# Kernel optimization log

Measured on AMD Instinct MI355X. Metric: run time of the kernel, lower is better.

The kernel has to match this reference:

```python
import jax, jax.numpy as jnp
import numpy as np

B, LTMS, TTS, C_IN, F, H = 64, 16, 256, 128, 256, 256


def setup_inputs() -> dict:
    key = jax.random.key(0)
    ks = jax.random.split(key, 6)
    s = 0.05  # small init keeps relu-GRU numerically tame
    return {
        "x": jax.random.normal(ks[0], (B, LTMS * TTS, C_IN), dtype=jnp.float32),
        "conv_w": jax.random.normal(ks[1], (1, C_IN, F), dtype=jnp.float32) * s,
        "conv_b": jnp.zeros((F,), dtype=jnp.float32),
        "attn_w": jax.random.normal(ks[2], (TTS, TTS), dtype=jnp.float32) * s,
        "attn_b": jnp.zeros((TTS,), dtype=jnp.float32),
        "gru_w": jax.random.normal(ks[3], (F, 3 * H), dtype=jnp.float32) * s,
        "gru_u": jax.random.normal(ks[4], (H, 3 * H), dtype=jnp.float32) * s,
        "gru_b": jnp.zeros((2, 3 * H), dtype=jnp.float32),
    }


def _forward(x, conv_w, conv_b, attn_w, attn_b, gru_w, gru_u, gru_b):
    b = x.shape[0]
    # [B, LTMS*TTS, C] -> [B*LTMS, TTS, C]; segments are independent, so the
    # original per-segment Python loop vectorizes into the leading batch dim.
    xs = x.reshape(b * LTMS, TTS, C_IN)
    # Conv1D kernel_size=1 == pointwise GEMM, then ReLU (dropout=0 at inference)
    conv = jax.nn.relu(jnp.einsum('ntc,cf->ntf', xs, conv_w[0]) + conv_b)  # [N,T,F]
    # Attention: softmax(Dense) over time axis per filter, multiply back
    xt = conv.transpose(0, 2, 1)                                  # [N,F,T]
    probs = jax.nn.softmax(xt @ attn_w + attn_b, axis=-1)         # [N,F,T]
    x_att = conv * probs.transpose(0, 2, 1)                       # [N,T,F]
    # GRU (keras v2, reset_after=True), activation=relu, gate order z,r,h
    bi, br = gru_b[0], gru_b[1]
    gates_x = x_att @ gru_w + bi                                  # [N,T,3H]
    def step(h, gx):
        rec = h @ gru_u + br
        xz, xr, xh = jnp.split(gx, 3, axis=-1)
        rz, rr, rh = jnp.split(rec, 3, axis=-1)
        z = jax.nn.sigmoid(xz + rz)
        r = jax.nn.sigmoid(xr + rr)
        hh = jax.nn.relu(xh + r * rh)
        h_new = z * h + (1.0 - z) * hh
        return h_new, None
    h0 = jnp.zeros((b * LTMS, H), dtype=x.dtype)
    h_final, _ = jax.lax.scan(step, h0, gates_x.transpose(1, 0, 2))
    return h_final.reshape(b, LTMS, H)


def reference(x, conv_w, conv_b, attn_w, attn_b, gru_w, gru_u, gru_b):
    return _forward(x, conv_w, conv_b, attn_w, attn_b, gru_w, gru_u, gru_b)
```

## Files before the change

kernel.cpp:

```cpp
#include <hip/hip_runtime.h>
#include <stdint.h>

typedef unsigned short u16;
typedef __attribute__((ext_vector_type(8))) __bf16 bf16x8;
typedef __attribute__((ext_vector_type(8))) u16 u16x8;
typedef __attribute__((ext_vector_type(4))) float f32x4;

#define TTS 256
#define NSEG 1024
#define TC 32

__device__ __forceinline__ u16 f2bf(float f) {
  union { float f; uint32_t u; } v; v.f = f;
  uint32_t r = v.u + 0x7fffu + ((v.u >> 16) & 1u);
  return (u16)(r >> 16);
}
__device__ __forceinline__ float bf2f(u16 h) {
  union { uint32_t u; float f; } v; v.u = ((uint32_t)h) << 16;
  return v.f;
}
__device__ __forceinline__ float sigm(float x) {
  return __builtin_amdgcn_rcpf(1.0f + __expf(-x));
}
__device__ __forceinline__ void gl16(const void* g, void* l) {
  __builtin_amdgcn_global_load_lds(
      (const __attribute__((address_space(1))) unsigned int*)g,
      (__attribute__((address_space(3))) unsigned int*)l, 16, 0, 0);
}

__global__ void k_transp4(const float* __restrict__ cw, const float* __restrict__ aw,
                          const float* __restrict__ gw, const float* __restrict__ gu,
                          u16* __restrict__ cwT, u16* __restrict__ awT,
                          u16* __restrict__ gwT, u16* __restrict__ guT) {
  int b = blockIdx.x;
  const float* in; u16* out; int R, C, base;
  if (b < 128)       { in = cw; out = cwT; R = 128; C = 256; base = 0; }
  else if (b < 384)  { in = aw; out = awT; R = 256; C = 256; base = 128; }
  else if (b < 1152) { in = gw; out = gwT; R = 256; C = 768; base = 384; }
  else               { in = gu; out = guT; R = 256; C = 768; base = 1152; }
  int i = (b - base) * 256 + threadIdx.x;
  if (i < R * C) {
    int r = i / C, c = i % C;
    out[(size_t)c * R + r] = f2bf(in[i]);
  }
}

template <bool RELU, bool STORE_T, int AMODE>
__global__ __launch_bounds__(512, 2) void k_gemm(
    const void* __restrict__ Av, const u16* __restrict__ Bt,
    const float* __restrict__ bias, u16* __restrict__ out, int K, int Nld, int t0) {
  __shared__ __attribute__((aligned(16))) u16 ldsA[2][4096];
  __shared__ __attribute__((aligned(16))) u16 ldsB[2][8192];
  __shared__ __attribute__((aligned(16))) u16 xw[STORE_T ? 8 * 16 * 70 : 16];
  const int tid  = threadIdx.x;
  const int w    = tid >> 6;
  const int lane = tid & 63;
  const int quad = lane >> 4;
  const int l16  = lane & 15;
  const int m0 = blockIdx.x * 128;
  const int n0 = blockIdx.y * 256;
  const int wm = w >> 2, wn = w & 3;
  const int srow = tid >> 2;
  const int scs  = (tid & 3) ^ (srow & 3);
  const int aslot = (srow * 4 + scs) * 8;
  const int xsw  = (quad ^ (l16 & 3)) * 8;
  const float* Af = (const float*)Av;
  const u16*   Ax = (const u16*)Av;

  f32x4 acc[4][4];
#pragma unroll
  for (int i = 0; i < 4; i++)
#pragma unroll
    for (int j = 0; j < 4; j++) acc[i][j] = f32x4{0.f, 0.f, 0.f, 0.f};

  float4 p0, p1;
  if (AMODE == 0) {
    const float* p = Af + (size_t)(m0 + srow) * K + (tid & 3) * 8;
    p0 = *(const float4*)p;
    p1 = *(const float4*)(p + 4);
  } else {
    int r = m0 + srow, kk = scs * 8;
    gl16(Ax + (size_t)(r >> 5) * 65536 + (size_t)(kk >> 6) * 16384 +
             (t0 + (r & 31)) * 64 + (kk & 63),
         &ldsA[0][tid * 8]);
  }
#pragma unroll
  for (int i = 0; i < 2; i++) {
    int idx = i * 512 + tid, brow = idx >> 2;
    int bcs = (idx & 3) ^ (brow & 3);
    gl16(Bt + (size_t)(n0 + brow) * K + bcs * 8, &ldsB[0][idx * 8]);
  }
  if (AMODE == 0) {
    *(ushort4*)&ldsA[0][aslot]     = ushort4{f2bf(p0.x), f2bf(p0.y), f2bf(p0.z), f2bf(p0.w)};
    *(ushort4*)&ldsA[0][aslot + 4] = ushort4{f2bf(p1.x), f2bf(p1.y), f2bf(p1.z), f2bf(p1.w)};
  }
  __syncthreads();

  int cur = 0;
  for (int k0 = 0; k0 < K; k0 += 32) {
    const int kn = k0 + 32;
    const bool more = kn < K;
    float4 q0, q1;
    if (more) {
      if (AMODE == 0) {
        const float* p = Af + (size_t)(m0 + srow) * K + kn + (tid & 3) * 8;
        q0 = *(const float4*)p;
        q1 = *(const float4*)(p + 4);
      } else {
        int r = m0 + srow, kk = kn + scs * 8;
        gl16(Ax + (size_t)(r >> 5) * 65536 + (size_t)(kk >> 6) * 16384 +
                 (t0 + (r & 31)) * 64 + (kk & 63),
             &ldsA[cur ^ 1][tid * 8]);
      }
#pragma unroll
      for (int i = 0; i < 2; i++) {
        int idx = i * 512 + tid, brow = idx >> 2;
        int bcs = (idx & 3) ^ (brow & 3);
        gl16(Bt + (size_t)(n0 + brow) * K + kn + bcs * 8, &ldsB[cur ^ 1][idx * 8]);
      }
    }
    bf16x8 a[4], b[4];
#pragma unroll
    for (int i = 0; i < 4; i++)
      a[i] = *(const bf16x8*)&ldsA[cur][(wm * 64 + i * 16 + l16) * 32 + xsw];
#pragma unroll
    for (int j = 0; j < 4; j++)
      b[j] = *(const bf16x8*)&ldsB[cur][(wn * 64 + j * 16 + l16) * 32 + xsw];
#pragma unroll
    for (int i = 0; i < 4; i++)
#pragma unroll
      for (int j = 0; j < 4; j++)
        acc[i][j] = __builtin_amdgcn_mfma_f32_16x16x32_bf16(a[i], b[j], acc[i][j], 0, 0, 0);
    if (AMODE == 0 && more) {
      *(ushort4*)&ldsA[cur ^ 1][aslot]     = ushort4{f2bf(q0.x), f2bf(q0.y), f2bf(q0.z), f2bf(q0.w)};
      *(ushort4*)&ldsA[cur ^ 1][aslot + 4] = ushort4{f2bf(q1.x), f2bf(q1.y), f2bf(q1.z), f2bf(q1.w)};
    }
    __syncthreads();
    cur ^= 1;
  }

  if (STORE_T) {
    const int nseg = m0 >> 8;
    const int ttw  = (m0 & 255) + wm * 64;
    const int col16 = lane >> 2, part = lane & 3;
    u16* xwp = &xw[w * 16 * 70];
#pragma unroll
    for (int j = 0; j < 4; j++) {
      int col = n0 + wn * 64 + j * 16 + l16;
      float bv = bias[col];
#pragma unroll
      for (int i = 0; i < 4; i++)
#pragma unroll
        for (int r = 0; r < 4; r++) {
          float v = acc[i][j][r] + bv;
          if (RELU) v = fmaxf(v, 0.f);
          xwp[l16 * 70 + i * 16 + quad * 4 + r] = f2bf(v);
        }
      u16x8 v0 = *(const u16x8*)&xwp[col16 * 70 + part * 16];
      u16x8 v1 = *(const u16x8*)&xwp[col16 * 70 + part * 16 + 8];
      int colS = n0 + wn * 64 + j * 16 + col16;
      size_t ob = (size_t)nseg * 65536 + (size_t)(colS >> 6) * 16384 +
                  (size_t)(colS & 63) * 256 + ttw + part * 16;
      *(u16x8*)&out[ob]     = v0;
      *(u16x8*)&out[ob + 8] = v1;
    }
  } else {
#pragma unroll
    for (int j = 0; j < 4; j++) {
      int col = n0 + wn * 64 + j * 16 + l16;
      float bv = bias[col];
#pragma unroll
      for (int i = 0; i < 4; i++) {
        int row0 = m0 + wm * 64 + i * 16 + quad * 4;
#pragma unroll
        for (int r = 0; r < 4; r++) {
          float v = acc[i][j][r] + bv;
          if (RELU) v = fmaxf(v, 0.f);
          out[(size_t)(row0 + r) * Nld + col] = f2bf(v);
        }
      }
    }
  }
}

__global__ __launch_bounds__(256, 3) void k_attn(
    u16* xac,
    const u16* __restrict__ Wt,
    const float* __restrict__ attn_b) {
  __shared__ __attribute__((aligned(16))) u16 ldsC[16384];
  __shared__ float redmax[4][64];
  __shared__ float redsum[4][64];
  __shared__ __attribute__((aligned(16))) u16 xbuf[4][16][76];
  const int tid  = threadIdx.x;
  const int w    = tid >> 6;
  const int lane = tid & 63;
  const int quad = lane >> 4;
  const int l16  = lane & 15;
  const int seg = blockIdx.x;
  const int c4  = blockIdx.y;
  u16* reg = xac + (size_t)seg * 65536 + (size_t)c4 * 16384;

#pragma unroll
  for (int u = 0; u < 8; u++) {
    int id = u * 256 + tid;
    int f = id >> 5;
    gl16(reg + ((id * 8) ^ ((f & 7) << 3)), &ldsC[id * 8]);
  }
  __syncthreads();

  f32x4 acc[4][4];
#pragma unroll
  for (int i = 0; i < 4; i++)
#pragma unroll
    for (int j = 0; j < 4; j++) acc[i][j] = f32x4{0.f, 0.f, 0.f, 0.f};

#pragma unroll
  for (int s = 0; s < 8; s++) {
    int k0 = s * 32;
    bf16x8 a[4], b[4];
#pragma unroll
    for (int i = 0; i < 4; i++)
      a[i] = *(const bf16x8*)(Wt + (size_t)(w * 64 + i * 16 + l16) * 256 + k0 + quad * 8);
#pragma unroll
    for (int j = 0; j < 4; j++) {
      int fl = j * 16 + l16;
      b[j] = *(const bf16x8*)&ldsC[(fl * 256 + s * 32 + quad * 8) ^ ((fl & 7) << 3)];
    }
#pragma unroll
    for (int i = 0; i < 4; i++)
#pragma unroll
      for (int j = 0; j < 4; j++)
        acc[i][j] = __builtin_amdgcn_mfma_f32_16x16x32_bf16(a[i], b[j], acc[i][j], 0, 0, 0);
  }

#pragma unroll
  for (int i = 0; i < 4; i++)
#pragma unroll
    for (int r = 0; r < 4; r++) {
      float ab = attn_b[w * 64 + i * 16 + quad * 4 + r];
#pragma unroll
      for (int j = 0; j < 4; j++) acc[i][j][r] += ab;
    }

  float lmax[4];
#pragma unroll
  for (int j = 0; j < 4; j++) {
    float m = -1e30f;
#pragma unroll
    for (int i = 0; i < 4; i++)
#pragma unroll
      for (int r = 0; r < 4; r++) m = fmaxf(m, acc[i][j][r]);
    m = fmaxf(m, __shfl_xor(m, 16));
    m = fmaxf(m, __shfl_xor(m, 32));
    lmax[j] = m;
  }
  if (quad == 0) {
#pragma unroll
    for (int j = 0; j < 4; j++) redmax[w][j * 16 + l16] = lmax[j];
  }
  __syncthreads();
  float gmax[4];
#pragma unroll
  for (int j = 0; j < 4; j++) {
    int c = j * 16 + l16;
    gmax[j] = fmaxf(fmaxf(redmax[0][c], redmax[1][c]), fmaxf(redmax[2][c], redmax[3][c]));
  }
  float lsum[4];
#pragma unroll
  for (int j = 0; j < 4; j++) {
    float sacc = 0.f;
#pragma unroll
    for (int i = 0; i < 4; i++)
#pragma unroll
      for (int r = 0; r < 4; r++) {
        float e = __expf(acc[i][j][r] - gmax[j]);
        acc[i][j][r] = e;
        sacc += e;
      }
    sacc += __shfl_xor(sacc, 16);
    sacc += __shfl_xor(sacc, 32);
    lsum[j] = sacc;
  }
  if (quad == 0) {
#pragma unroll
    for (int j = 0; j < 4; j++) redsum[w][j * 16 + l16] = lsum[j];
  }
  __syncthreads();
  float rinv[4];
#pragma unroll
  for (int j = 0; j < 4; j++) {
    int c = j * 16 + l16;
    rinv[j] = 1.0f / (redsum[0][c] + redsum[1][c] + redsum[2][c] + redsum[3][c]);
  }

#pragma unroll
  for (int i = 0; i < 4; i++) {
#pragma unroll
    for (int r = 0; r < 4; r++) {
      int tp = w * 64 + i * 16 + quad * 4 + r;
#pragma unroll
      for (int j = 0; j < 4; j++) {
        int fl = j * 16 + l16;
        float cv = bf2f(ldsC[(fl * 256 + tp) ^ ((fl & 7) << 3)]);
        float xa = acc[i][j][r] * rinv[j] * cv;
        xbuf[w][quad * 4 + r][fl] = f2bf(xa);
      }
    }
    int rr = lane >> 2, oc = lane & 3;
    u16x8 v0 = *(const u16x8*)&xbuf[w][rr][oc * 16];
    u16x8 v1 = *(const u16x8*)&xbuf[w][rr][oc * 16 + 8];
    int tpb = w * 64 + i * 16 + rr;
    *(u16x8*)&reg[(size_t)tpb * 64 + oc * 16]     = v0;
    *(u16x8*)&reg[(size_t)tpb * 64 + oc * 16 + 8] = v1;
  }
}

__global__ __launch_bounds__(512) __attribute__((amdgpu_waves_per_eu(2, 2)))
void k_scan(
    const u16* __restrict__ gc,
    const u16* __restrict__ Ut,
    const float* __restrict__ br,
    float* __restrict__ hio,
    int init) {
  __shared__ __attribute__((aligned(16))) u16 hbT[2][4096];
  __shared__ __attribute__((aligned(16))) u16 ldsG[2][12288];
  const int tid  = threadIdx.x;
  const int w    = tid >> 6;
  const int lane = tid & 63;
  const int quad = lane >> 4;
  const int l16  = lane & 15;
  const int n0 = blockIdx.x * 16;
  const int cg[2] = {w, 8 + w};

  bf16x8 U[2][3][8];
#pragma unroll
  for (int grp = 0; grp < 2; grp++)
#pragma unroll
    for (int g = 0; g < 3; g++)
#pragma unroll
      for (int s = 0; s < 8; s++) {
        U[grp][g][s] = *(const bf16x8*)(Ut + (size_t)(g * 256 + cg[grp] * 16 + l16) * 256 + s * 32 + quad * 8);
        asm volatile("" : "+v"(U[grp][g][s]));
      }

  float brZ[2], brR[2], brH[2];
#pragma unroll
  for (int grp = 0; grp < 2; grp++) {
    int c = cg[grp] * 16 + l16;
    brZ[grp] = br[c]; brR[grp] = br[256 + c]; brH[grp] = br[512 + c];
  }

  int gbase[2], hwb[2];
#pragma unroll
  for (int grp = 0; grp < 2; grp++) {
    gbase[grp] = cg[grp] * 256 + quad * 16 + l16;
    int c = cg[grp] * 16 + l16;
    hwb[grp] = (c >> 5) * 512 + ((c >> 3) & 3) * 128 + (c & 7) + quad * 32;
  }
  const int ahb = quad * 128 + l16 * 8;

  float hreg[2][4];
#pragma unroll
  for (int grp = 0; grp < 2; grp++)
#pragma unroll
    for (int r = 0; r < 4; r++) {
      hreg[grp][r] = init ? 0.f
                          : hio[(size_t)(n0 + quad * 4 + r) * 256 + cg[grp] * 16 + l16];
      hbT[0][hwb[grp] + r * 8] = f2bf(hreg[grp][r]);
    }

  const u16* sp[3];
#pragma unroll
  for (int k = 0; k < 3; k++) {
    int id = tid + k * 512;
    int a = id & 1, q = (id >> 1) & 3, r = (id >> 3) & 3;
    int cgv = (id >> 5) & 15, g = id >> 9;
    sp[k] = gc + ((size_t)(n0 + q * 4 + r) * 32 + 0) * 768 + g * 256 + cgv * 16 + a * 8;
  }
#pragma unroll
  for (int k = 0; k < 3; k++) {
    gl16(sp[k], &ldsG[0][(tid + k * 512) * 8]);
    sp[k] += 768;
  }
  __syncthreads();

  for (int tt = 0; tt < TC; tt++) {
    if (tt + 1 < TC) {
#pragma unroll
      for (int k = 0; k < 3; k++) {
        gl16(sp[k], &ldsG[(tt + 1) & 1][(tid + k * 512) * 8]);
        sp[k] += 768;
      }
    }

    f32x4 acc[2][3];
#pragma unroll
    for (int grp = 0; grp < 2; grp++)
#pragma unroll
      for (int g = 0; g < 3; g++) acc[grp][g] = f32x4{0.f, 0.f, 0.f, 0.f};

    const u16* hR = hbT[tt & 1];
#pragma unroll
    for (int s = 0; s < 8; s++) {
      bf16x8 ah = *(const bf16x8*)&hR[ahb + s * 512];
#pragma unroll
      for (int grp = 0; grp < 2; grp++)
#pragma unroll
        for (int g = 0; g < 3; g++)
          acc[grp][g] = __builtin_amdgcn_mfma_f32_16x16x32_bf16(ah, U[grp][g][s], acc[grp][g], 0, 0, 0);
    }

    const u16* G = ldsG[tt & 1];
    u16* hW = hbT[(tt + 1) & 1];
#pragma unroll
    for (int grp = 0; grp < 2; grp++)
#pragma unroll
      for (int r = 0; r < 4; r++) {
        float gz = bf2f(G[gbase[grp] + 0 * 4096 + r * 64]);
        float gr = bf2f(G[gbase[grp] + 1 * 4096 + r * 64]);
        float gh = bf2f(G[gbase[grp] + 2 * 4096 + r * 64]);
        float z  = sigm(acc[grp][0][r] + gz + brZ[grp]);
        float rg = sigm(acc[grp][1][r] + gr + brR[grp]);
        float hh = fmaxf(gh + rg * (acc[grp][2][r] + brH[grp]), 0.f);
        float hn = z * hreg[grp][r] + (1.0f - z) * hh;
        hreg[grp][r] = hn;
        hW[hwb[grp] + r * 8] = f2bf(hn);
      }
    __syncthreads();
  }

#pragma unroll
  for (int grp = 0; grp < 2; grp++)
#pragma unroll
    for (int r = 0; r < 4; r++)
      hio[(size_t)(n0 + quad * 4 + r) * 256 + cg[grp] * 16 + l16] = hreg[grp][r];
}

extern "C" void kernel_launch(void* const* d_in, const int* in_sizes, int n_in,
                              void* d_out, int out_size, void* d_ws, size_t ws_size,
                              hipStream_t stream) {
  (void)in_sizes; (void)n_in; (void)out_size;
  const float* x      = (const float*)d_in[0];
  const float* conv_w = (const float*)d_in[1];
  const float* conv_b = (const float*)d_in[2];
  const float* attn_w = (const float*)d_in[3];
  const float* attn_b = (const float*)d_in[4];
  const float* gru_w  = (const float*)d_in[5];
  const float* gru_u  = (const float*)d_in[6];
  const float* gru_b  = (const float*)d_in[7];

  const size_t NEEDED = 185532416;
  if (ws_size < NEEDED) return;
  char* ws = (char*)d_ws;
  u16* xac     = (u16*)(ws);
  u16* gatesC  = (u16*)(ws + 134217728);
  u16* conv_wT = (u16*)(ws + 184549376);
  u16* attn_wT = (u16*)(ws + 184614912);
  u16* gru_wT  = (u16*)(ws + 184745984);
  u16* gru_uT  = (u16*)(ws + 185139200);

  hipLaunchKernelGGL(k_transp4, dim3(1920), dim3(256), 0, stream,
                     conv_w, attn_w, gru_w, gru_u, conv_wT, attn_wT, gru_wT, gru_uT);

  hipLaunchKernelGGL((k_gemm<true, true, 0>), dim3(2048, 1), dim3(512), 0, stream,
                     (const void*)x, conv_wT, conv_b, xac, 128, 0, 0);
  hipLaunchKernelGGL(k_attn, dim3(1024, 4), dim3(256), 0, stream,
                     xac, attn_wT, attn_b);
  for (int c = 0; c < 8; c++) {
    hipLaunchKernelGGL((k_gemm<false, false, 1>), dim3(256, 3), dim3(512), 0, stream,
                       (const void*)xac, gru_wT, gru_b, gatesC, 256, 768, c * TC);
    hipLaunchKernelGGL(k_scan, dim3(64), dim3(512), 0, stream,
                       gatesC, gru_uT, gru_b + 768, (float*)d_out, c == 0 ? 1 : 0);
  }
}
```

Baseline: 1.122 ms.

## Deepen scan gate prefetch to 3 stages with explicit vmcnt waits and swizzled layout

The GRU scan kernel's gate prefetch ring grows from double to quadruple buffering, running three timesteps ahead. The plain __syncthreads is replaced by explicit vmcnt/lgkmcnt waits plus s_barrier, so loads still in flight need not drain every step. The gate tile is now copied row-contiguously with an XOR swizzle to cut LDS bank conflicts on reads. The attention launch is also split into two half-grid launches, which adds launch overhead without an obvious benefit.

```diff
diff --git a/kernel.cpp b/kernel.cpp
--- a/kernel.cpp
+++ b/kernel.cpp
@@ -9,6 +9,10 @@
 #define TTS 256
 #define NSEG 1024
 #define TC 32
+
+#define WAITV(N) asm volatile("s_waitcnt vmcnt(" #N ")" ::: "memory")
+#define LGKM0    asm volatile("s_waitcnt lgkmcnt(0)" ::: "memory")
+#define SBAR     do { __builtin_amdgcn_s_barrier(); __builtin_amdgcn_sched_barrier(0); } while (0)
 
 __device__ __forceinline__ u16 f2bf(float f) {
   union { float f; uint32_t u; } v; v.f = f;
@@ -186,7 +190,7 @@
 __global__ __launch_bounds__(256, 3) void k_attn(
     u16* xac,
     const u16* __restrict__ Wt,
-    const float* __restrict__ attn_b) {
+    const float* __restrict__ attn_b, int seg0) {
   __shared__ __attribute__((aligned(16))) u16 ldsC[16384];
   __shared__ float redmax[4][64];
   __shared__ float redsum[4][64];
@@ -196,7 +200,7 @@
   const int lane = tid & 63;
   const int quad = lane >> 4;
   const int l16  = lane & 15;
-  const int seg = blockIdx.x;
+  const int seg = blockIdx.x + seg0;
   const int c4  = blockIdx.y;
   u16* reg = xac + (size_t)seg * 65536 + (size_t)c4 * 16384;
 
@@ -323,7 +327,7 @@
     float* __restrict__ hio,
     int init) {
   __shared__ __attribute__((aligned(16))) u16 hbT[2][4096];
-  __shared__ __attribute__((aligned(16))) u16 ldsG[2][12288];
+  __shared__ __attribute__((aligned(16))) u16 ldsG[4][12288];
   const int tid  = threadIdx.x;
   const int w    = tid >> 6;
   const int lane = tid & 63;
@@ -350,10 +354,10 @@
     brZ[grp] = br[c]; brR[grp] = br[256 + c]; brH[grp] = br[512 + c];
   }
 
-  int gbase[2], hwb[2];
+  int csw[2], hwb[2];
 #pragma unroll
   for (int grp = 0; grp < 2; grp++) {
-    gbase[grp] = cg[grp] * 256 + quad * 16 + l16;
+    csw[grp] = (cg[grp] * 16 + l16) ^ (quad << 4);
     int c = cg[grp] * 16 + l16;
     hwb[grp] = (c >> 5) * 512 + ((c >> 3) & 3) * 128 + (c & 7) + quad * 32;
   }
@@ -373,22 +377,27 @@
 #pragma unroll
   for (int k = 0; k < 3; k++) {
     int id = tid + k * 512;
-    int a = id & 1, q = (id >> 1) & 3, r = (id >> 3) & 3;
-    int cgv = (id >> 5) & 15, g = id >> 9;
-    sp[k] = gc + ((size_t)(n0 + q * 4 + r) * 32 + 0) * 768 + g * 256 + cgv * 16 + a * 8;
-  }
-#pragma unroll
-  for (int k = 0; k < 3; k++) {
-    gl16(sp[k], &ldsG[0][(tid + k * 512) * 8]);
-    sp[k] += 768;
-  }
-  __syncthreads();
+    int row = id / 96, col16 = id - row * 96;
+    int sw = ((row >> 2) & 3) << 4;
+    sp[k] = gc + (size_t)(n0 + row) * TC * 768 + ((col16 * 8) ^ sw);
+  }
+#pragma unroll
+  for (int p = 0; p < 3; p++) {
+#pragma unroll
+    for (int k = 0; k < 3; k++) {
+      gl16(sp[k], &ldsG[p][(tid + k * 512) * 8]);
+      sp[k] += 768;
+    }
+  }
+  WAITV(6);
+  LGKM0;
+  SBAR;
 
   for (int tt = 0; tt < TC; tt++) {
-    if (tt + 1 < TC) {
+    if (tt < TC - 3) {
 #pragma unroll
       for (int k = 0; k < 3; k++) {
-        gl16(sp[k], &ldsG[(tt + 1) & 1][(tid + k * 512) * 8]);
+        gl16(sp[k], &ldsG[(tt + 3) & 3][(tid + k * 512) * 8]);
         sp[k] += 768;
       }
     }
@@ -410,15 +419,16 @@
           acc[grp][g] = __builtin_amdgcn_mfma_f32_16x16x32_bf16(ah, U[grp][g][s], acc[grp][g], 0, 0, 0);
     }
 
-    const u16* G = ldsG[tt & 1];
+    const u16* G = ldsG[tt & 3];
     u16* hW = hbT[(tt + 1) & 1];
 #pragma unroll
     for (int grp = 0; grp < 2; grp++)
 #pragma unroll
       for (int r = 0; r < 4; r++) {
-        float gz = bf2f(G[gbase[grp] + 0 * 4096 + r * 64]);
-        float gr = bf2f(G[gbase[grp] + 1 * 4096 + r * 64]);
-        float gh = bf2f(G[gbase[grp] + 2 * 4096 + r * 64]);
+        int rb = (quad * 4 + r) * 768 + csw[grp];
+        float gz = bf2f(G[rb]);
+        float gr = bf2f(G[rb + 256]);
+        float gh = bf2f(G[rb + 512]);
         float z  = sigm(acc[grp][0][r] + gz + brZ[grp]);
         float rg = sigm(acc[grp][1][r] + gr + brR[grp]);
         float hh = fmaxf(gh + rg * (acc[grp][2][r] + brH[grp]), 0.f);
@@ -426,7 +436,12 @@
         hreg[grp][r] = hn;
         hW[hwb[grp] + r * 8] = f2bf(hn);
       }
-    __syncthreads();
+
+    if (tt < TC - 3)      { WAITV(6); }
+    else if (tt == TC - 3){ WAITV(3); }
+    else if (tt == TC - 2){ WAITV(0); }
+    LGKM0;
+    SBAR;
   }
 
 #pragma unroll
@@ -464,8 +479,10 @@
 
   hipLaunchKernelGGL((k_gemm<true, true, 0>), dim3(2048, 1), dim3(512), 0, stream,
                      (const void*)x, conv_wT, conv_b, xac, 128, 0, 0);
-  hipLaunchKernelGGL(k_attn, dim3(1024, 4), dim3(256), 0, stream,
-                     xac, attn_wT, attn_b);
+  hipLaunchKernelGGL(k_attn, dim3(512, 4), dim3(256), 0, stream,
+                     xac, attn_wT, attn_b, 0);
+  hipLaunchKernelGGL(k_attn, dim3(512, 4), dim3(256), 0, stream,
+                     xac, attn_wT, attn_b, 512);
   for (int c = 0; c < 8; c++) {
     hipLaunchKernelGGL((k_gemm<false, false, 1>), dim3(256, 3), dim3(512), 0, stream,
                        (const void*)xac, gru_wT, gru_b, gatesC, 256, 768, c * TC);
```

Result: slower. 1.249 ms (+11.4%).
